# Kernel optimization log

Hardware: AMD Instinct MI355X
Metric: run time of the kernel (lower is better)

The kernel has to match this reference:

```python
import jax, jax.numpy as jnp
import numpy as np

B, N, DIN = 1, 1024, 512
NF, DCOND, H = 4, 128, 8
HD = DIN // H


def layernorm(x, g, b, eps=1e-5):
    mu = jnp.mean(x, axis=-1, keepdims=True)
    var = jnp.var(x, axis=-1, keepdims=True)
    return (x - mu) * jax.lax.rsqrt(var + eps) * g + b


def modlin2d(x, code, w_c, ln_g, ln_b, W, b):
    # code: [dcond, nf]; w_c: [din, dcond] -> code_mod: [nf, 1, din]
    code_mod = layernorm((w_c @ code).T, ln_g, ln_b)[:, None, :]
    return jnp.matmul(x * code_mod, W.T) + b


def setup_inputs() -> dict:
    key = jax.random.key(0)
    ks = jax.random.split(key, 8)
    s = lambda d: 1.0 / np.sqrt(d)
    return {
        "x": jax.random.normal(ks[0], (B, N, DIN), jnp.float32),
        "compatibility": jax.random.uniform(ks[1], (B, NF, N), jnp.float32),
        "code": jax.random.normal(ks[2], (DCOND, NF), jnp.float32),
        "w_c": jax.random.normal(ks[3], (DIN, DCOND), jnp.float32) * s(DCOND),
        "W_qkv": jax.random.normal(ks[4], (3 * DIN, DIN), jnp.float32) * s(DIN),
        "b_qkv": jnp.zeros((3 * DIN,), jnp.float32),
        "W_proj": jax.random.normal(ks[5], (DIN, DIN), jnp.float32) * s(DIN),
        "b_proj": jnp.zeros((DIN,), jnp.float32),
        "ln_qkv_g": jnp.ones((DIN,), jnp.float32),
        "ln_qkv_b": jnp.zeros((DIN,), jnp.float32),
        "ln_proj_g": jnp.ones((DIN,), jnp.float32),
        "ln_proj_b": jnp.zeros((DIN,), jnp.float32),
    }


def reference(x, compatibility, code, w_c, W_qkv, b_qkv, W_proj, b_proj,
              ln_qkv_g, ln_qkv_b, ln_proj_g, ln_proj_b):
    b, n, e = x.shape
    hd = e // H
    scale = hd ** -0.5
    # QKV: [B, nf, N, 3*din] -> split into [3, B, H, nf, N, hd]
    qkv = modlin2d(x[:, None, :, :], code, w_c, ln_qkv_g, ln_qkv_b, W_qkv, b_qkv)
    qkv = qkv.reshape(b, NF, n, 3, H, hd).transpose(3, 0, 4, 1, 2, 5)
    q, k, v = qkv[0], qkv[1], qkv[2]
    # first softmax over scaled scores
    attn = jax.nn.softmax(jnp.einsum('bhfnd,bhfmd->bhfnm', q, k) * scale, axis=-1)
    # compatibility outer product: [B, N, N] (sums over function axis)
    compat = jnp.einsum('bfn,bfm->bnm', compatibility, compatibility)
    W_hat = attn * compat[:, None, None, :, :]
    # second softmax
    Wm = jax.nn.softmax(W_hat, axis=-1)
    y_hat = jnp.einsum('bhfnm,bhfmd->bhfnd', Wm, v)
    y_hat = y_hat.transpose(0, 2, 3, 1, 4).reshape(b, NF, n, e)
    y = modlin2d(y_hat, code, w_c, ln_proj_g, ln_proj_b, W_proj, b_proj)
    return y
```

## Files before the change

### kernel.cpp

```cpp
#include <hip/hip_runtime.h>
#include <hip/hip_bf16.h>
#include <math.h>

#define NTOK 1024
#define DIN  512
#define NF   4
#define DCOND 128
#define H    8
#define HD   64
#define NQKV 1536

typedef __attribute__((ext_vector_type(8))) short bf16x8;
typedef __attribute__((ext_vector_type(4))) float f32x4;
typedef __attribute__((ext_vector_type(4))) unsigned short us4;

__device__ __forceinline__ unsigned short f2b(float f) {
  union { float f; unsigned int u; } v; v.f = f;
  unsigned int r = v.u + 0x7fffu + ((v.u >> 16) & 1u);
  return (unsigned short)(r >> 16);
}

__device__ __forceinline__ float b2f(unsigned short h) {
  union { unsigned int u; float f; } v; v.u = ((unsigned int)h) << 16;
  return v.f;
}

__device__ __forceinline__ float asf(unsigned int u) {
  union { unsigned int u; float f; } v; v.u = u;
  return v.f;
}

__device__ __forceinline__ void gl_lds16(const void* g, void* l) {
  __builtin_amdgcn_global_load_lds(
      (const __attribute__((address_space(1))) unsigned int*)g,
      (__attribute__((address_space(3))) unsigned int*)l, 16, 0, 0);
}

__global__ void ln_kernel(const float* __restrict__ code, const float* __restrict__ w_c,
                          const float* __restrict__ lnqg, const float* __restrict__ lnqb,
                          const float* __restrict__ lnpg, const float* __restrict__ lnpb,
                          float* __restrict__ cmq, float* __restrict__ cmp_) {
  const int i = threadIdx.x;
  const int w = i >> 6, lane = i & 63;
  float t[NF] = {0.f, 0.f, 0.f, 0.f};
  const float* wr = w_c + i * DCOND;
#pragma unroll 8
  for (int k = 0; k < DCOND; k += 4) {
    float4 wv = *reinterpret_cast<const float4*>(wr + k);
    float4 c0 = *reinterpret_cast<const float4*>(&code[k * 4]);
    float4 c1 = *reinterpret_cast<const float4*>(&code[(k + 1) * 4]);
    float4 c2 = *reinterpret_cast<const float4*>(&code[(k + 2) * 4]);
    float4 c3 = *reinterpret_cast<const float4*>(&code[(k + 3) * 4]);
    t[0] += wv.x * c0.x + wv.y * c1.x + wv.z * c2.x + wv.w * c3.x;
    t[1] += wv.x * c0.y + wv.y * c1.y + wv.z * c2.y + wv.w * c3.y;
    t[2] += wv.x * c0.z + wv.y * c1.z + wv.z * c2.z + wv.w * c3.z;
    t[3] += wv.x * c0.w + wv.y * c1.w + wv.z * c2.w + wv.w * c3.w;
  }
  __shared__ float redS[8], redQ[8];
#pragma unroll
  for (int f = 0; f < NF; ++f) {
    float s = t[f], q = t[f] * t[f];
#pragma unroll
    for (int o = 32; o > 0; o >>= 1) { s += __shfl_xor(s, o); q += __shfl_xor(q, o); }
    if (lane == 0) { redS[w] = s; redQ[w] = q; }
    __syncthreads();
    float S = 0.f, Q = 0.f;
#pragma unroll
    for (int j = 0; j < 8; ++j) { S += redS[j]; Q += redQ[j]; }
    float mu = S * (1.f / 512.f);
    float var = Q * (1.f / 512.f) - mu * mu;
    float rstd = rsqrtf(var + 1e-5f);
    float nv = (t[f] - mu) * rstd;
    cmq[f * DIN + i]  = nv * lnqg[i] + lnqb[i];
    cmp_[f * DIN + i] = nv * lnpg[i] + lnpb[i];
    __syncthreads();
  }
}

__global__ void prep2_kernel(const float* __restrict__ W_qkv, const float* __restrict__ W_proj,
                             const float* __restrict__ x, const float* __restrict__ cmq,
                             unsigned short* __restrict__ Wqh, unsigned short* __restrict__ Wph,
                             unsigned short* __restrict__ xm) {
  const int bid = blockIdx.x, tid = threadIdx.x;
  if (bid < 256) {
    const float* src; unsigned short* dst; int e;
    if (bid < 192) { src = W_qkv; dst = Wqh; e = bid * 4096 + tid * 16; }
    else { src = W_proj; dst = Wph; e = (bid - 192) * 4096 + tid * 16; }
#pragma unroll
    for (int j = 0; j < 4; ++j) {
      float4 a = *reinterpret_cast<const float4*>(&src[e + j * 4]);
      us4 p = { f2b(a.x), f2b(a.y), f2b(a.z), f2b(a.w) };
      *reinterpret_cast<us4*>(&dst[e + j * 4]) = p;
    }
  } else {
    int e = (bid - 256) * 4096 + tid * 16;
    int row = e >> 9, d = e & 511;
    int f = row >> 10, n = row & 1023;
    const float* xr = x + (size_t)n * DIN + d;
    const float* cr = cmq + f * DIN + d;
#pragma unroll
    for (int j = 0; j < 4; ++j) {
      float4 a = *reinterpret_cast<const float4*>(xr + j * 4);
      float4 c = *reinterpret_cast<const float4*>(cr + j * 4);
      us4 p = { f2b(a.x * c.x), f2b(a.y * c.y), f2b(a.z * c.z), f2b(a.w * c.w) };
      *reinterpret_cast<us4*>(&xm[e + j * 4]) = p;
    }
  }
}

template<int NCOL, bool OUT_BF16, bool WRITE_VT, bool SCALE_Q>
__global__ __launch_bounds__(256, 6)
void gemm64(const unsigned short* __restrict__ Ah,
            const unsigned short* __restrict__ Wh,
            const float* __restrict__ bias,
            unsigned short* __restrict__ outH,
            float* __restrict__ outF,
            unsigned short* __restrict__ vT) {
  __shared__ __align__(16) unsigned short sA[2][2048];
  __shared__ __align__(16) unsigned short sB[2][2048];
  const int tid = threadIdx.x;
  const int lane = tid & 63, w = tid >> 6;
  const int li = lane & 15, g = lane >> 4;
  const int wr = (w >> 1) * 32, wc = (w & 1) * 32;
  const int row0 = blockIdx.y * 64, col0 = blockIdx.x * 64;
  const int f = row0 >> 10;
  const int sr = tid >> 2, sp = tid & 3;
  const int ss = sp ^ ((sr >> 1) & 3);

  f32x4 acc[2][2];
#pragma unroll
  for (int m = 0; m < 2; ++m)
#pragma unroll
    for (int n = 0; n < 2; ++n) acc[m][n] = (f32x4){0.f, 0.f, 0.f, 0.f};

  const unsigned short* aSrc = Ah + (size_t)(row0 + sr) * DIN + ss * 8;
  const unsigned short* bSrc = Wh + (size_t)(col0 + sr) * DIN + ss * 8;

  gl_lds16(aSrc, &sA[0][w * 512]);
  gl_lds16(bSrc, &sB[0][w * 512]);
  __syncthreads();
  for (int it = 0; it < 16; ++it) {
    int buf = it & 1;
    if (it < 15) {
      gl_lds16(aSrc + (it + 1) * 32, &sA[buf ^ 1][w * 512]);
      gl_lds16(bSrc + (it + 1) * 32, &sB[buf ^ 1][w * 512]);
    }
    bf16x8 aF[2], bF[2];
#pragma unroll
    for (int m = 0; m < 2; ++m) {
      int ra = wr + m * 16 + li;
      aF[m] = *reinterpret_cast<const bf16x8*>(&sA[buf][(ra * 4 + (g ^ ((ra >> 1) & 3))) * 8]);
    }
#pragma unroll
    for (int n = 0; n < 2; ++n) {
      int cb = wc + n * 16 + li;
      bF[n] = *reinterpret_cast<const bf16x8*>(&sB[buf][(cb * 4 + (g ^ ((cb >> 1) & 3))) * 8]);
    }
#pragma unroll
    for (int m = 0; m < 2; ++m)
#pragma unroll
      for (int n = 0; n < 2; ++n)
        acc[m][n] = __builtin_amdgcn_mfma_f32_16x16x32_bf16(aF[m], bF[n], acc[m][n], 0, 0, 0);
    __syncthreads();
  }
#pragma unroll
  for (int n = 0; n < 2; ++n) {
    int col = col0 + wc + n * 16 + li;
    float bb = bias[col];
    float sc = (SCALE_Q && col < DIN) ? 0.125f : 1.0f;
#pragma unroll
    for (int m = 0; m < 2; ++m) {
      int rb = row0 + wr + m * 16 + g * 4;
      f32x4 v = acc[m][n];
      if constexpr (OUT_BF16) {
        if (WRITE_VT && col >= 1024) {
          int tok0 = rb & 1023;
          us4 pk;
#pragma unroll
          for (int r = 0; r < 4; ++r) pk[r] = f2b(v[r] + bb);
          *reinterpret_cast<us4*>(&vT[((size_t)(f * 512 + (col - 1024))) * NTOK + tok0]) = pk;
        } else {
#pragma unroll
          for (int r = 0; r < 4; ++r)
            outH[(size_t)(rb + r) * NCOL + col] = f2b((v[r] + bb) * sc);
        }
      } else {
#pragma unroll
        for (int r = 0; r < 4; ++r)
          outF[(size_t)(rb + r) * NCOL + col] = v[r] + bb;
      }
    }
  }
}

__global__ __launch_bounds__(256, 3)
void attn_mfma2(const unsigned short* __restrict__ qkvh,
                const unsigned short* __restrict__ vTh,
                const float* __restrict__ comp,
                const float* __restrict__ cmp_,
                unsigned short* __restrict__ ym) {
  __shared__ __align__(16) unsigned short sK[2][4096];
  __shared__ __align__(16) unsigned short sV[2][4096];
  __shared__ __align__(16) unsigned short sW[4][16 * 72];
  __shared__ unsigned int sc01[1024], sc23[1024];
  __shared__ float lred[2][2][16];
  __shared__ float s2red[2][16];
  const int tid = threadIdx.x, lane = tid & 63, w = tid >> 6;
  const int li = lane & 15, g = lane >> 4;
  const int rt = w & 1, ch = w >> 1;
  const int hf = blockIdx.x, qt = blockIdx.y;
  const int h = hf >> 2, f = hf & 3;

  {
    int c = tid * 4;
    float4 a0 = *reinterpret_cast<const float4*>(&comp[c]);
    float4 a1 = *reinterpret_cast<const float4*>(&comp[1024 + c]);
    float4 a2 = *reinterpret_cast<const float4*>(&comp[2048 + c]);
    float4 a3 = *reinterpret_cast<const float4*>(&comp[3072 + c]);
    sc01[c + 0] = f2b(a0.x) | ((unsigned int)f2b(a1.x) << 16);
    sc01[c + 1] = f2b(a0.y) | ((unsigned int)f2b(a1.y) << 16);
    sc01[c + 2] = f2b(a0.z) | ((unsigned int)f2b(a1.z) << 16);
    sc01[c + 3] = f2b(a0.w) | ((unsigned int)f2b(a1.w) << 16);
    sc23[c + 0] = f2b(a2.x) | ((unsigned int)f2b(a3.x) << 16);
    sc23[c + 1] = f2b(a2.y) | ((unsigned int)f2b(a3.y) << 16);
    sc23[c + 2] = f2b(a2.z) | ((unsigned int)f2b(a3.z) << 16);
    sc23[c + 3] = f2b(a2.w) | ((unsigned int)f2b(a3.w) << 16);
  }

  const int qrow0 = qt * 32 + rt * 16;
  const unsigned short* qbase = qkvh + ((size_t)(f * NTOK + qrow0 + li)) * NQKV + h * HD;
  bf16x8 aq[2];
  aq[0] = *reinterpret_cast<const bf16x8*>(qbase + g * 8);
  aq[1] = *reinterpret_cast<const bf16x8*>(qbase + 32 + g * 8);

  float crow[4][4];
#pragma unroll
  for (int ff = 0; ff < 4; ++ff)
#pragma unroll
    for (int r = 0; r < 4; ++r)
      crow[ff][r] = comp[ff * NTOK + qrow0 + g * 4 + r];

  const unsigned short* kb = qkvh + ((size_t)(f * NTOK)) * NQKV + DIN + h * HD;
  const unsigned short* vb = vTh + ((size_t)(f * DIN + h * HD)) * NTOK;

  auto stageK = [&](unsigned short* dst, int t) {
#pragma unroll
    for (int j = 0; j < 8; ++j) {
      int slot = j * 64 + lane;
      int tok = slot >> 3, sp = slot & 7, s = sp ^ (tok & 7);
      gl_lds16(kb + (size_t)(t * 64 + tok) * NQKV + s * 8, dst + j * 512);
    }
  };
  auto stageV = [&](unsigned short* dst, int t) {
#pragma unroll
    for (int j = 0; j < 8; ++j) {
      int slot = j * 64 + lane;
      int d = slot >> 3, sp = slot & 7, s = sp ^ (d & 7);
      gl_lds16(vb + (size_t)d * NTOK + t * 64 + s * 8, dst + j * 512);
    }
  };

  float lsum[4] = {0.f, 0.f, 0.f, 0.f};
  stageK(sK[ch], ch * 8);
  __syncthreads();
  for (int tt = 0; tt < 8; ++tt) {
    unsigned short* cur = (tt & 1) ? sV[ch] : sK[ch];
    if (tt < 7) {
      unsigned short* nxt = (tt & 1) ? sK[ch] : sV[ch];
      stageK(nxt, ch * 8 + tt + 1);
    }
    bf16x8 bk[4][2];
#pragma unroll
    for (int cf = 0; cf < 4; ++cf)
#pragma unroll
      for (int ks = 0; ks < 2; ++ks) {
        int tok = cf * 16 + li, s = ks * 4 + g;
        bk[cf][ks] = *reinterpret_cast<const bf16x8*>(&cur[(tok * 8 + (s ^ (tok & 7))) * 8]);
      }
    f32x4 accs[4];
#pragma unroll
    for (int cf = 0; cf < 4; ++cf) accs[cf] = (f32x4){0.f, 0.f, 0.f, 0.f};
#pragma unroll
    for (int ks = 0; ks < 2; ++ks)
#pragma unroll
      for (int cf = 0; cf < 4; ++cf)
        accs[cf] = __builtin_amdgcn_mfma_f32_16x16x32_bf16(aq[ks], bk[cf][ks], accs[cf], 0, 0, 0);
#pragma unroll
    for (int cf = 0; cf < 4; ++cf)
#pragma unroll
      for (int r = 0; r < 4; ++r) lsum[r] += __expf(accs[cf][r]);
    __syncthreads();
  }
#pragma unroll
  for (int r = 0; r < 4; ++r) {
    lsum[r] += __shfl_xor(lsum[r], 1);
    lsum[r] += __shfl_xor(lsum[r], 2);
    lsum[r] += __shfl_xor(lsum[r], 4);
    lsum[r] += __shfl_xor(lsum[r], 8);
  }
  if (li == 0) {
#pragma unroll
    for (int r = 0; r < 4; ++r) lred[ch][rt][g * 4 + r] = lsum[r];
  }
  __syncthreads();
  float invl[4];
#pragma unroll
  for (int r = 0; r < 4; ++r)
    invl[r] = 1.f / (lred[0][rt][g * 4 + r] + lred[1][rt][g * 4 + r]);

  f32x4 acco[4];
  float sum2[4] = {0.f, 0.f, 0.f, 0.f};
#pragma unroll
  for (int cf = 0; cf < 4; ++cf) acco[cf] = (f32x4){0.f, 0.f, 0.f, 0.f};
  unsigned short* wbuf = &sW[w][0];

  for (int tt = 0; tt < 8; ++tt) {
    int t = ch * 8 + tt;
    stageK(sK[ch], t);
    stageV(sV[ch], t);
    __syncthreads();
    bf16x8 bk[4][2];
#pragma unroll
    for (int cf = 0; cf < 4; ++cf)
#pragma unroll
      for (int ks = 0; ks < 2; ++ks) {
        int tok = cf * 16 + li, s = ks * 4 + g;
        bk[cf][ks] = *reinterpret_cast<const bf16x8*>(&sK[ch][(tok * 8 + (s ^ (tok & 7))) * 8]);
      }
    f32x4 accs[4];
#pragma unroll
    for (int cf = 0; cf < 4; ++cf) accs[cf] = (f32x4){0.f, 0.f, 0.f, 0.f};
#pragma unroll
    for (int ks = 0; ks < 2; ++ks)
#pragma unroll
      for (int cf = 0; cf < 4; ++cf)
        accs[cf] = __builtin_amdgcn_mfma_f32_16x16x32_bf16(aq[ks], bk[cf][ks], accs[cf], 0, 0, 0);
#pragma unroll
    for (int cf = 0; cf < 4; ++cf) {
      int colg = t * 64 + cf * 16 + li;
      unsigned int u01 = sc01[colg], u23 = sc23[colg];
      float c0 = asf(u01 << 16), c1 = asf(u01 & 0xffff0000u);
      float c2 = asf(u23 << 16), c3 = asf(u23 & 0xffff0000u);
#pragma unroll
      for (int r = 0; r < 4; ++r) {
        float a = __expf(accs[cf][r]) * invl[r];
        float cc = crow[0][r] * c0 + crow[1][r] * c1 + crow[2][r] * c2 + crow[3][r] * c3;
        float tv = __expf(a * cc);
        unsigned short hv = f2b(tv);
        sum2[r] += b2f(hv);
        wbuf[(g * 4 + r) * 72 + cf * 16 + li] = hv;
      }
    }
    bf16x8 aw[2], bv2[4][2];
#pragma unroll
    for (int ks = 0; ks < 2; ++ks)
      aw[ks] = *reinterpret_cast<const bf16x8*>(&wbuf[li * 72 + ks * 32 + g * 8]);
#pragma unroll
    for (int cf = 0; cf < 4; ++cf)
#pragma unroll
      for (int ks = 0; ks < 2; ++ks) {
        int d = cf * 16 + li, s = ks * 4 + g;
        bv2[cf][ks] = *reinterpret_cast<const bf16x8*>(&sV[ch][(d * 8 + (s ^ (d & 7))) * 8]);
      }
#pragma unroll
    for (int ks = 0; ks < 2; ++ks)
#pragma unroll
      for (int cf = 0; cf < 4; ++cf)
        acco[cf] = __builtin_amdgcn_mfma_f32_16x16x32_bf16(aw[ks], bv2[cf][ks], acco[cf], 0, 0, 0);
    __syncthreads();
  }

#pragma unroll
  for (int r = 0; r < 4; ++r) {
    sum2[r] += __shfl_xor(sum2[r], 1);
    sum2[r] += __shfl_xor(sum2[r], 2);
    sum2[r] += __shfl_xor(sum2[r], 4);
    sum2[r] += __shfl_xor(sum2[r], 8);
  }
  float* fred = (float*)sK;
  if (ch == 1) {
    if (li == 0) {
#pragma unroll
      for (int r = 0; r < 4; ++r) s2red[rt][g * 4 + r] = sum2[r];
    }
#pragma unroll
    for (int cf = 0; cf < 4; ++cf)
#pragma unroll
      for (int r = 0; r < 4; ++r)
        fred[rt * 1024 + (g * 4 + r) * 64 + cf * 16 + li] = acco[cf][r];
  }
  __syncthreads();
  if (ch == 0) {
    float invs[4];
#pragma unroll
    for (int r = 0; r < 4; ++r) invs[r] = 1.f / (sum2[r] + s2red[rt][g * 4 + r]);
    float cscale[4];
#pragma unroll
    for (int cf = 0; cf < 4; ++cf) cscale[cf] = cmp_[f * DIN + h * HD + cf * 16 + li];
#pragma unroll
    for (int cf = 0; cf < 4; ++cf)
#pragma unroll
      for (int r = 0; r < 4; ++r) {
        float v = (acco[cf][r] + fred[rt * 1024 + (g * 4 + r) * 64 + cf * 16 + li]) * invs[r];
        int qrow = qrow0 + g * 4 + r;
        ym[((size_t)(f * NTOK + qrow)) * DIN + h * HD + cf * 16 + li] = f2b(v * cscale[cf]);
      }
  }
}

extern "C" void kernel_launch(void* const* d_in, const int* in_sizes, int n_in,
                              void* d_out, int out_size, void* d_ws, size_t ws_size,
                              hipStream_t stream) {
  const float* x      = (const float*)d_in[0];
  const float* compat = (const float*)d_in[1];
  const float* code   = (const float*)d_in[2];
  const float* w_c    = (const float*)d_in[3];
  const float* W_qkv  = (const float*)d_in[4];
  const float* b_qkv  = (const float*)d_in[5];
  const float* W_proj = (const float*)d_in[6];
  const float* b_proj = (const float*)d_in[7];
  const float* lnqg   = (const float*)d_in[8];
  const float* lnqb   = (const float*)d_in[9];
  const float* lnpg   = (const float*)d_in[10];
  const float* lnpb   = (const float*)d_in[11];
  float* out = (float*)d_out;

  float* cmq  = (float*)d_ws;
  float* cmp_ = cmq + NF * DIN;
  unsigned short* Wqh  = (unsigned short*)(cmp_ + NF * DIN);
  unsigned short* Wph  = Wqh + (size_t)NQKV * DIN;
  unsigned short* xm   = Wph + (size_t)DIN * DIN;
  unsigned short* qkvh = xm + (size_t)NF * NTOK * DIN;
  unsigned short* vTh  = qkvh + (size_t)NF * NTOK * NQKV;
  unsigned short* ym   = vTh + (size_t)NF * DIN * NTOK;

  ln_kernel<<<1, 512, 0, stream>>>(code, w_c, lnqg, lnqb, lnpg, lnpb, cmq, cmp_);
  prep2_kernel<<<768, 256, 0, stream>>>(W_qkv, W_proj, x, cmq, Wqh, Wph, xm);
  gemm64<NQKV, true, true, true><<<dim3(24, 64), 256, 0, stream>>>(
      xm, Wqh, b_qkv, qkvh, nullptr, vTh);
  attn_mfma2<<<dim3(32, 32), 256, 0, stream>>>(qkvh, vTh, compat, cmp_, ym);
  gemm64<DIN, false, false, false><<<dim3(8, 64), 256, 0, stream>>>(
      ym, Wph, b_proj, nullptr, out, nullptr);
}
```

Before: 173.7 us.

## Widen attention blocks to 64 query rows with shared K/V staging and exp2

The attention kernel now runs 512 threads per block covering 64 query rows instead of 32, so each staged K/V tile serves twice as many rows and total global K/V traffic per head drops. Staging is spread across all eight waves, and a block-wide barrier is added around each stage. The log2(e) factor is folded into the Q scale and the softmax normalizer so native exp2 replaces __expf. The cost is fewer blocks (512 instead of 1024), an extra barrier per iteration in the second pass, and no overlap of loads with compute in that pass.

```diff
diff --git a/kernel.cpp b/kernel.cpp
--- a/kernel.cpp
+++ b/kernel.cpp
@@ -9,6 +9,7 @@
 #define H    8
 #define HD   64
 #define NQKV 1536
+#define LOG2E 1.4426950408889634f
 
 typedef __attribute__((ext_vector_type(8))) short bf16x8;
 typedef __attribute__((ext_vector_type(4))) float f32x4;
@@ -167,7 +168,7 @@
   for (int n = 0; n < 2; ++n) {
     int col = col0 + wc + n * 16 + li;
     float bb = bias[col];
-    float sc = (SCALE_Q && col < DIN) ? 0.125f : 1.0f;
+    float sc = (SCALE_Q && col < DIN) ? (0.125f * LOG2E) : 1.0f;
 #pragma unroll
     for (int m = 0; m < 2; ++m) {
       int rb = row0 + wr + m * 16 + g * 4;
@@ -193,41 +194,38 @@
   }
 }
 
-__global__ __launch_bounds__(256, 3)
-void attn_mfma2(const unsigned short* __restrict__ qkvh,
+__global__ __launch_bounds__(512, 4)
+void attn_mfma4(const unsigned short* __restrict__ qkvh,
                 const unsigned short* __restrict__ vTh,
                 const float* __restrict__ comp,
                 const float* __restrict__ cmp_,
                 unsigned short* __restrict__ ym) {
   __shared__ __align__(16) unsigned short sK[2][4096];
   __shared__ __align__(16) unsigned short sV[2][4096];
-  __shared__ __align__(16) unsigned short sW[4][16 * 72];
+  __shared__ __align__(16) unsigned short wbuf_all[8][16 * 68];
   __shared__ unsigned int sc01[1024], sc23[1024];
-  __shared__ float lred[2][2][16];
-  __shared__ float s2red[2][16];
+  __shared__ float lred[2][4][16];
+  __shared__ float s2red[4][16];
+
   const int tid = threadIdx.x, lane = tid & 63, w = tid >> 6;
   const int li = lane & 15, g = lane >> 4;
-  const int rt = w & 1, ch = w >> 1;
+  const int rt = w & 3, ch = w >> 2;
   const int hf = blockIdx.x, qt = blockIdx.y;
   const int h = hf >> 2, f = hf & 3;
 
   {
-    int c = tid * 4;
-    float4 a0 = *reinterpret_cast<const float4*>(&comp[c]);
-    float4 a1 = *reinterpret_cast<const float4*>(&comp[1024 + c]);
-    float4 a2 = *reinterpret_cast<const float4*>(&comp[2048 + c]);
-    float4 a3 = *reinterpret_cast<const float4*>(&comp[3072 + c]);
-    sc01[c + 0] = f2b(a0.x) | ((unsigned int)f2b(a1.x) << 16);
+    int c = tid * 2;
+    float2 a0 = *reinterpret_cast<const float2*>(&comp[c]);
+    float2 a1 = *reinterpret_cast<const float2*>(&comp[1024 + c]);
+    float2 a2 = *reinterpret_cast<const float2*>(&comp[2048 + c]);
+    float2 a3 = *reinterpret_cast<const float2*>(&comp[3072 + c]);
+    sc01[c]     = f2b(a0.x) | ((unsigned int)f2b(a1.x) << 16);
     sc01[c + 1] = f2b(a0.y) | ((unsigned int)f2b(a1.y) << 16);
-    sc01[c + 2] = f2b(a0.z) | ((unsigned int)f2b(a1.z) << 16);
-    sc01[c + 3] = f2b(a0.w) | ((unsigned int)f2b(a1.w) << 16);
-    sc23[c + 0] = f2b(a2.x) | ((unsigned int)f2b(a3.x) << 16);
+    sc23[c]     = f2b(a2.x) | ((unsigned int)f2b(a3.x) << 16);
     sc23[c + 1] = f2b(a2.y) | ((unsigned int)f2b(a3.y) << 16);
-    sc23[c + 2] = f2b(a2.z) | ((unsigned int)f2b(a3.z) << 16);
-    sc23[c + 3] = f2b(a2.w) | ((unsigned int)f2b(a3.w) << 16);
-  }
-
-  const int qrow0 = qt * 32 + rt * 16;
+  }
+
+  const int qrow0 = qt * 64 + rt * 16;
   const unsigned short* qbase = qkvh + ((size_t)(f * NTOK + qrow0 + li)) * NQKV + h * HD;
   bf16x8 aq[2];
   aq[0] = *reinterpret_cast<const bf16x8*>(qbase + g * 8);
@@ -243,39 +241,39 @@
   const unsigned short* kb = qkvh + ((size_t)(f * NTOK)) * NQKV + DIN + h * HD;
   const unsigned short* vb = vTh + ((size_t)(f * DIN + h * HD)) * NTOK;
 
-  auto stageK = [&](unsigned short* dst, int t) {
-#pragma unroll
-    for (int j = 0; j < 8; ++j) {
-      int slot = j * 64 + lane;
-      int tok = slot >> 3, sp = slot & 7, s = sp ^ (tok & 7);
-      gl_lds16(kb + (size_t)(t * 64 + tok) * NQKV + s * 8, dst + j * 512);
+  const int remK = w * 64 + lane;
+  const int ktok = remK >> 3, kdg = remK & 7;
+  const int ksw = kdg ^ (ktok & 7);
+
+  auto stageK_to = [&](unsigned short (*dst)[4096], int s) {
+#pragma unroll
+    for (int j = 0; j < 2; ++j) {
+      int tokg = j * 512 + s * 64 + ktok;
+      gl_lds16(kb + (size_t)tokg * NQKV + ksw * 8, &dst[j][(w * 64) * 8]);
     }
   };
-  auto stageV = [&](unsigned short* dst, int t) {
-#pragma unroll
-    for (int j = 0; j < 8; ++j) {
-      int slot = j * 64 + lane;
-      int d = slot >> 3, sp = slot & 7, s = sp ^ (d & 7);
-      gl_lds16(vb + (size_t)d * NTOK + t * 64 + s * 8, dst + j * 512);
+  auto stageV_to = [&](int s) {
+#pragma unroll
+    for (int j = 0; j < 2; ++j) {
+      int d = ktok, tg = kdg;
+      int sw = tg ^ (d & 7);
+      gl_lds16(vb + (size_t)d * NTOK + j * 512 + s * 64 + sw * 8, &sV[j][(w * 64) * 8]);
     }
   };
 
   float lsum[4] = {0.f, 0.f, 0.f, 0.f};
-  stageK(sK[ch], ch * 8);
-  __syncthreads();
-  for (int tt = 0; tt < 8; ++tt) {
-    unsigned short* cur = (tt & 1) ? sV[ch] : sK[ch];
-    if (tt < 7) {
-      unsigned short* nxt = (tt & 1) ? sK[ch] : sV[ch];
-      stageK(nxt, ch * 8 + tt + 1);
-    }
+  stageK_to(sK, 0);
+  __syncthreads();
+  for (int s = 0; s < 8; ++s) {
+    unsigned short (*cur)[4096] = (s & 1) ? sV : sK;
+    if (s < 7) stageK_to((s & 1) ? sK : sV, s + 1);
     bf16x8 bk[4][2];
 #pragma unroll
     for (int cf = 0; cf < 4; ++cf)
 #pragma unroll
       for (int ks = 0; ks < 2; ++ks) {
-        int tok = cf * 16 + li, s = ks * 4 + g;
-        bk[cf][ks] = *reinterpret_cast<const bf16x8*>(&cur[(tok * 8 + (s ^ (tok & 7))) * 8]);
+        int tok = cf * 16 + li, dg = ks * 4 + g;
+        bk[cf][ks] = *reinterpret_cast<const bf16x8*>(&cur[ch][(tok * 8 + (dg ^ (tok & 7))) * 8]);
       }
     f32x4 accs[4];
 #pragma unroll
@@ -288,7 +286,7 @@
 #pragma unroll
     for (int cf = 0; cf < 4; ++cf)
 #pragma unroll
-      for (int r = 0; r < 4; ++r) lsum[r] += __expf(accs[cf][r]);
+      for (int r = 0; r < 4; ++r) lsum[r] += __builtin_amdgcn_exp2f(accs[cf][r]);
     __syncthreads();
   }
 #pragma unroll
@@ -306,26 +304,25 @@
   float invl[4];
 #pragma unroll
   for (int r = 0; r < 4; ++r)
-    invl[r] = 1.f / (lred[0][rt][g * 4 + r] + lred[1][rt][g * 4 + r]);
+    invl[r] = LOG2E / (lred[0][rt][g * 4 + r] + lred[1][rt][g * 4 + r]);
 
   f32x4 acco[4];
   float sum2[4] = {0.f, 0.f, 0.f, 0.f};
 #pragma unroll
   for (int cf = 0; cf < 4; ++cf) acco[cf] = (f32x4){0.f, 0.f, 0.f, 0.f};
-  unsigned short* wbuf = &sW[w][0];
-
-  for (int tt = 0; tt < 8; ++tt) {
-    int t = ch * 8 + tt;
-    stageK(sK[ch], t);
-    stageV(sV[ch], t);
-    __syncthreads();
+  unsigned short* wb = wbuf_all[w];
+
+  stageK_to(sK, 0);
+  stageV_to(0);
+  __syncthreads();
+  for (int s = 0; s < 8; ++s) {
     bf16x8 bk[4][2];
 #pragma unroll
     for (int cf = 0; cf < 4; ++cf)
 #pragma unroll
       for (int ks = 0; ks < 2; ++ks) {
-        int tok = cf * 16 + li, s = ks * 4 + g;
-        bk[cf][ks] = *reinterpret_cast<const bf16x8*>(&sK[ch][(tok * 8 + (s ^ (tok & 7))) * 8]);
+        int tok = cf * 16 + li, dg = ks * 4 + g;
+        bk[cf][ks] = *reinterpret_cast<const bf16x8*>(&sK[ch][(tok * 8 + (dg ^ (tok & 7))) * 8]);
       }
     f32x4 accs[4];
 #pragma unroll
@@ -337,36 +334,39 @@
         accs[cf] = __builtin_amdgcn_mfma_f32_16x16x32_bf16(aq[ks], bk[cf][ks], accs[cf], 0, 0, 0);
 #pragma unroll
     for (int cf = 0; cf < 4; ++cf) {
-      int colg = t * 64 + cf * 16 + li;
+      int colg = ch * 512 + s * 64 + cf * 16 + li;
       unsigned int u01 = sc01[colg], u23 = sc23[colg];
       float c0 = asf(u01 << 16), c1 = asf(u01 & 0xffff0000u);
       float c2 = asf(u23 << 16), c3 = asf(u23 & 0xffff0000u);
 #pragma unroll
       for (int r = 0; r < 4; ++r) {
-        float a = __expf(accs[cf][r]) * invl[r];
+        float e = __builtin_amdgcn_exp2f(accs[cf][r]);
+        float a = e * invl[r];
         float cc = crow[0][r] * c0 + crow[1][r] * c1 + crow[2][r] * c2 + crow[3][r] * c3;
-        float tv = __expf(a * cc);
+        float tv = __builtin_amdgcn_exp2f(a * cc);
         unsigned short hv = f2b(tv);
         sum2[r] += b2f(hv);
-        wbuf[(g * 4 + r) * 72 + cf * 16 + li] = hv;
-      }
-    }
-    bf16x8 aw[2], bv2[4][2];
+        wb[(g * 4 + r) * 68 + cf * 16 + li] = hv;
+      }
+    }
+    bf16x8 aw[2], bv[4][2];
 #pragma unroll
     for (int ks = 0; ks < 2; ++ks)
-      aw[ks] = *reinterpret_cast<const bf16x8*>(&wbuf[li * 72 + ks * 32 + g * 8]);
+      aw[ks] = *reinterpret_cast<const bf16x8*>(&wb[li * 68 + ks * 32 + g * 8]);
 #pragma unroll
     for (int cf = 0; cf < 4; ++cf)
 #pragma unroll
       for (int ks = 0; ks < 2; ++ks) {
-        int d = cf * 16 + li, s = ks * 4 + g;
-        bv2[cf][ks] = *reinterpret_cast<const bf16x8*>(&sV[ch][(d * 8 + (s ^ (d & 7))) * 8]);
+        int d = cf * 16 + li, tg = ks * 4 + g;
+        bv[cf][ks] = *reinterpret_cast<const bf16x8*>(&sV[ch][(d * 8 + (tg ^ (d & 7))) * 8]);
       }
 #pragma unroll
     for (int ks = 0; ks < 2; ++ks)
 #pragma unroll
       for (int cf = 0; cf < 4; ++cf)
-        acco[cf] = __builtin_amdgcn_mfma_f32_16x16x32_bf16(aw[ks], bv2[cf][ks], acco[cf], 0, 0, 0);
+        acco[cf] = __builtin_amdgcn_mfma_f32_16x16x32_bf16(aw[ks], bv[cf][ks], acco[cf], 0, 0, 0);
+    __syncthreads();
+    if (s < 7) { stageK_to(sK, s + 1); stageV_to(s + 1); }
     __syncthreads();
   }
 
@@ -378,6 +378,7 @@
     sum2[r] += __shfl_xor(sum2[r], 8);
   }
   float* fred = (float*)sK;
+  __syncthreads();
   if (ch == 1) {
     if (li == 0) {
 #pragma unroll
@@ -438,7 +439,7 @@
   prep2_kernel<<<768, 256, 0, stream>>>(W_qkv, W_proj, x, cmq, Wqh, Wph, xm);
   gemm64<NQKV, true, true, true><<<dim3(24, 64), 256, 0, stream>>>(
       xm, Wqh, b_qkv, qkvh, nullptr, vTh);
-  attn_mfma2<<<dim3(32, 32), 256, 0, stream>>>(qkvh, vTh, compat, cmp_, ym);
+  attn_mfma4<<<dim3(32, 16), 512, 0, stream>>>(qkvh, vTh, compat, cmp_, ym);
   gemm64<DIN, false, false, false><<<dim3(8, 64), 256, 0, stream>>>(
       ym, Wph, b_proj, nullptr, out, nullptr);
 }
```

After: 163.4 us. 5.9% less time.
